# Kernel tuning notes

Hardware: AMD Instinct MI355X
Metric: run time of the kernel (lower is better)

Reference implementation:

```python
import jax, jax.numpy as jnp
import numpy as np
import math

E = 4096  # embed_dim
H = 32    # num_heads
M = 256   # max_queries
B = 8     # batch
N = 256   # kv tokens (16x16 grid -> no pos-embed interpolation branch)


def _sincos_1d(d, pos):
    omega = np.arange(d // 2, dtype=np.float32) / (d / 2.0)
    omega = 1.0 / 10000 ** omega
    out = np.einsum('m,d->md', pos.reshape(-1), omega)
    return np.concatenate([np.sin(out), np.cos(out)], axis=1)


def _sincos_2d(embed_dim, grid_size):
    gh = np.arange(grid_size, dtype=np.float32)
    gw = np.arange(grid_size, dtype=np.float32)
    grid = np.stack(np.meshgrid(gw, gh), axis=0).reshape(2, -1)
    return np.concatenate([
        _sincos_1d(embed_dim // 2, grid[0]),
        _sincos_1d(embed_dim // 2, grid[1]),
    ], axis=1)


def setup_inputs() -> dict:
    key = jax.random.key(0)
    ks = jax.random.split(key, 4)
    grid_size = int(math.ceil(math.sqrt(M)))
    pe = _sincos_2d(E, grid_size)[:M].astype(np.float32)
    return {
        'x': jax.random.normal(ks[0], (B, N, E), jnp.float32),
        'query': 0.02 * jax.random.normal(ks[1], (M, E), jnp.float32),
        'pos_embed': jnp.asarray(pe),
        'ln_q_w': jnp.ones((E,), jnp.float32),
        'ln_q_b': jnp.zeros((E,), jnp.float32),
        'ln_kv_w': jnp.ones((E,), jnp.float32),
        'ln_kv_b': jnp.zeros((E,), jnp.float32),
        'in_proj_w': 0.02 * jax.random.normal(ks[2], (3 * E, E), jnp.float32),
        'in_proj_b': jnp.zeros((3 * E,), jnp.float32),
        'out_proj_w': 0.02 * jax.random.normal(ks[3], (E, E), jnp.float32),
        'out_proj_b': jnp.zeros((E,), jnp.float32),
    }


def _ln(x, w, b, eps=1e-5):
    m = jnp.mean(x, -1, keepdims=True)
    v = jnp.mean((x - m) ** 2, -1, keepdims=True)
    return (x - m) * jax.lax.rsqrt(v + eps) * w + b


def reference(x, query, pos_embed, ln_q_w, ln_q_b, ln_kv_w, ln_kv_b,
              in_proj_w, in_proj_b, out_proj_w, out_proj_b):
    D = E // H
    kv = _ln(x, ln_kv_w, ln_kv_b)                      # [B,N,E] (kv_proj is Identity)
    q_in = _ln(query, ln_q_w, ln_q_b) + pos_embed      # [M,E] (Q + posQ, shared over batch)
    k_in = kv + pos_embed[None]                        # N == M so posK == pos_embed (no interp)
    Wq, Wk, Wv = in_proj_w[:E], in_proj_w[E:2 * E], in_proj_w[2 * E:]
    bq, bk, bv = in_proj_b[:E], in_proj_b[E:2 * E], in_proj_b[2 * E:]
    q = (q_in @ Wq.T + bq).reshape(M, H, D).transpose(1, 0, 2)          # [H,M,D]
    k = (k_in @ Wk.T + bk).reshape(B, N, H, D).transpose(0, 2, 1, 3)    # [B,H,N,D]
    v = (kv @ Wv.T + bv).reshape(B, N, H, D).transpose(0, 2, 1, 3)      # [B,H,N,D]
    scores = jnp.einsum('hmd,bhnd->bhmn', q, k) / jnp.sqrt(jnp.float32(D))
    attn = jax.nn.softmax(scores, axis=-1)                              # [B,H,M,N]
    o = jnp.einsum('bhmn,bhnd->bhmd', attn, v)
    o = o.transpose(0, 2, 1, 3).reshape(B, M, E)
    out = o @ out_proj_w.T + out_proj_b                                 # [B,M,E]
    # need_weights=True with average_attn_weights=True -> head-averaged weights
    return out, attn.mean(axis=1)
```

## Files before the change

kernel.cpp:

```cpp
#include <hip/hip_runtime.h>
#include <hip/hip_bf16.h>

typedef __bf16 bf16;
typedef __attribute__((ext_vector_type(8))) __bf16 bf16x8;
typedef __attribute__((ext_vector_type(4))) __bf16 bf16x4;
typedef __attribute__((ext_vector_type(4))) float floatx4;

#define E_DIM 4096
#define H_DIM 32
#define D_DIM 128
#define M_DIM 256
#define B_DIM 8
#define N_DIM 256

#define GLD_LDS(g, l) __builtin_amdgcn_global_load_lds( \
    (const __attribute__((address_space(1))) unsigned int*)(g), \
    (__attribute__((address_space(3))) unsigned int*)(l), 16, 0, 0)

__device__ __forceinline__ float wave_sum(float v) {
#pragma unroll
  for (int o = 32; o; o >>= 1) v += __shfl_xor(v, o);
  return v;
}
__device__ __forceinline__ float wave_max(float v) {
#pragma unroll
  for (int o = 32; o; o >>= 1) v = fmaxf(v, __shfl_xor(v, o));
  return v;
}

#define BAR256() asm volatile("s_barrier" ::: "memory")
#define LGKM0_256()                                      \
  asm volatile("s_waitcnt lgkmcnt(0)" ::: "memory");     \
  __builtin_amdgcn_sched_barrier(0)

#define STAGE_A256(T, h)                                                       \
  {                                                                            \
    _Pragma("unroll") for (int j = 0; j < 2; ++j)                              \
        GLD_LDS(Ag + (size_t)((h)*128 + sgrow + j * 8) * lda + (T) * 64 + sgcol, \
                AsP + ((T)&1) * 16384 + (h)*8192 + sdst + j * 512);            \
  }
#define STAGE_B256(T, h)                                                       \
  {                                                                            \
    _Pragma("unroll") for (int j = 0; j < 2; ++j)                              \
        GLD_LDS(Bg + (size_t)((h)*128 + sgrow + j * 8) * ldb + (T) * 64 + sgcol, \
                BsP + ((T)&1) * 16384 + (h)*8192 + sdst + j * 512);            \
  }
#define LDA256(mh)                                                             \
  {                                                                            \
    _Pragma("unroll") for (int m = 0; m < 4; ++m) {                            \
      a[m][0] = *(const bf16x8*)(AsP + buf + rA + ((mh)*4 + m) * 1024 + slot0); \
      a[m][1] = *(const bf16x8*)(AsP + buf + rA + ((mh)*4 + m) * 1024 + slot1); \
    }                                                                          \
  }
#define LDB256(dst, nh)                                                        \
  {                                                                            \
    _Pragma("unroll") for (int n = 0; n < 2; ++n) {                            \
      dst[n][0] = *(const bf16x8*)(BsP + buf + rB + ((nh)*2 + n) * 1024 + slot0); \
      dst[n][1] = *(const bf16x8*)(BsP + buf + rB + ((nh)*2 + n) * 1024 + slot1); \
    }                                                                          \
  }
#define MFMAQ(mb, nb, B)                                                       \
  {                                                                            \
    _Pragma("unroll") for (int m = 0; m < 4; ++m)                              \
        _Pragma("unroll") for (int n = 0; n < 2; ++n) {                        \
      acc[(mb) + m][(nb) + n] = __builtin_amdgcn_mfma_f32_16x16x32_bf16(       \
          a[m][0], B[n][0], acc[(mb) + m][(nb) + n], 0, 0, 0);                 \
      acc[(mb) + m][(nb) + n] = __builtin_amdgcn_mfma_f32_16x16x32_bf16(       \
          a[m][1], B[n][1], acc[(mb) + m][(nb) + n], 0, 0, 0);                 \
    }                                                                          \
  }

__device__ __forceinline__ void gemm256_core(const bf16* __restrict__ Ag,
                                             const bf16* __restrict__ Bg,
                                             int lda, int ldb, int nkt,
                                             bf16* AsP, bf16* BsP,
                                             floatx4 (&acc)[8][4],
                                             int wid, int lane) {
  const int wm = wid >> 2, wn = wid & 3;
  const int l15 = lane & 15, q = lane >> 4, e7 = lane & 7;
  const int slot0 = ((q ^ e7) & 7) * 8;
  const int slot1 = (((4 + q) ^ e7) & 7) * 8;
  const int rA = (wm * 128 + l15) * 64;
  const int rB = (wn * 64 + l15) * 64;
  const int sgrow = wid * 16 + (lane >> 3);
  const int sgcol = ((lane & 7) ^ (lane >> 3)) * 8;
  const int sdst = wid * 1024;

  bf16x8 a[4][2], b0[2][2], b1[2][2];

  STAGE_B256(0, 0); STAGE_B256(0, 1);
  STAGE_A256(0, 0); STAGE_A256(0, 1);
  STAGE_B256(1, 0); STAGE_B256(1, 1);

  for (int U = 0; U < nkt; ++U) {
    const int buf = (U & 1) * 16384;
    if (U + 1 < nkt)
      asm volatile("s_waitcnt vmcnt(4)\n\ts_barrier" ::: "memory");
    else
      asm volatile("s_waitcnt vmcnt(0)\n\ts_barrier" ::: "memory");
    LDA256(0); LDB256(b0, 0);
    if (U + 1 < nkt) { STAGE_A256(U + 1, 0); }
    BAR256(); LGKM0_256();
    __builtin_amdgcn_s_setprio(1); MFMAQ(0, 0, b0); __builtin_amdgcn_s_setprio(0);
    __builtin_amdgcn_sched_barrier(0); BAR256();
    LDB256(b1, 1);
    if (U + 1 < nkt) { STAGE_A256(U + 1, 1); }
    BAR256(); LGKM0_256();
    __builtin_amdgcn_s_setprio(1); MFMAQ(0, 2, b1); __builtin_amdgcn_s_setprio(0);
    __builtin_amdgcn_sched_barrier(0); BAR256();
    LDA256(1);
    if (U + 2 < nkt) { STAGE_B256(U + 2, 0); }
    BAR256(); LGKM0_256();
    __builtin_amdgcn_s_setprio(1); MFMAQ(4, 2, b1); __builtin_amdgcn_s_setprio(0);
    __builtin_amdgcn_sched_barrier(0); BAR256();
    if (U + 2 < nkt) { STAGE_B256(U + 2, 1); }
    BAR256();
    __builtin_amdgcn_s_setprio(1); MFMAQ(4, 0, b0); __builtin_amdgcn_s_setprio(0);
    __builtin_amdgcn_sched_barrier(0);
  }
}

__global__ __launch_bounds__(512, 1)
void proj256(const bf16* __restrict__ qin, const bf16* __restrict__ kin,
             const bf16* __restrict__ kv, const bf16* __restrict__ Wqkv,
             const float* __restrict__ bqkv, float* __restrict__ qpart,
             bf16* __restrict__ kp, bf16* __restrict__ vt) {
  __shared__ __align__(16) bf16 As2[32768];
  __shared__ __align__(16) bf16 Bs2[32768];
  const int tid = threadIdx.x, wid = tid >> 6, lane = tid & 63;

  const int o = blockIdx.x;
  const int id = (o & 7) * 32 + (o >> 3);
  int role, bx, by;
  const bf16 *A, *B;
  const float* bias;
  bf16* C;
  if (id < 128) {
    role = 1; by = id & 7; bx = id >> 3;
    A = kin; B = Wqkv + 16777216; bias = bqkv + 4096; C = kp;
  } else {
    role = 2; by = (id - 128) & 7; bx = (id - 128) >> 3;
    A = kv; B = Wqkv + 33554432; bias = bqkv + 8192; C = vt;
  }
  const int trowA = by * 256, trowB = bx * 256;
  const bf16* Ag = A + (size_t)trowA * E_DIM;
  const bf16* Bg = B + (size_t)trowB * E_DIM;

  floatx4 acc[8][4];
#pragma unroll
  for (int i = 0; i < 8; ++i)
#pragma unroll
    for (int j = 0; j < 4; ++j) acc[i][j] = (floatx4){0.f, 0.f, 0.f, 0.f};

  gemm256_core(Ag, Bg, E_DIM, E_DIM, 64, As2, Bs2, acc, wid, lane);

  const int wm = wid >> 2, wn = wid & 3;
  const int l15 = lane & 15, q = lane >> 4;
  const int mrow0 = trowA + wm * 128 + q * 4;
  const int ncol0 = trowB + wn * 64 + l15;
  if (role == 1) {
#pragma unroll
    for (int m = 0; m < 8; ++m)
#pragma unroll
      for (int n = 0; n < 4; ++n) {
        const int col = ncol0 + n * 16;
        const float bb = bias[col];
        floatx4 v = acc[m][n];
#pragma unroll
        for (int r = 0; r < 4; ++r)
          C[(size_t)(mrow0 + m * 16 + r) * E_DIM + col] = (bf16)(v[r] + bb);
      }
  } else {
#pragma unroll
    for (int m = 0; m < 8; ++m)
#pragma unroll
      for (int n = 0; n < 4; ++n) {
        const int col = ncol0 + n * 16;
        const int h = col >> 7, d = col & 127;
        const float bb = bias[col];
        const int row0 = mrow0 + m * 16;
        const int b_ = row0 >> 8, n_ = row0 & 255;
        floatx4 v = acc[m][n];
        bf16x4 p;
#pragma unroll
        for (int r = 0; r < 4; ++r) p[r] = (bf16)(v[r] + bb);
        *(bf16x4*)(C + ((size_t)((b_ * H_DIM + h) * D_DIM + d)) * N_DIM + n_) = p;
      }
  }

  const int qx = id & 15, kc = id >> 4;
  const bf16* Agq = qin + kc * 256;
  const bf16* Bgq = Wqkv + (size_t)(qx * 256) * E_DIM + kc * 256;
#pragma unroll
  for (int i = 0; i < 8; ++i)
#pragma unroll
    for (int j = 0; j < 4; ++j) acc[i][j] = (floatx4){0.f, 0.f, 0.f, 0.f};

  gemm256_core(Agq, Bgq, E_DIM, E_DIM, 4, As2, Bs2, acc, wid, lane);

  float* qdst = qpart + (size_t)kc * 1048576;
  const int qmrow0 = wm * 128 + q * 4;
  const int qncol0 = qx * 256 + wn * 64 + l15;
#pragma unroll
  for (int m = 0; m < 8; ++m)
#pragma unroll
    for (int n = 0; n < 4; ++n) {
      const int col = qncol0 + n * 16;
      floatx4 v = acc[m][n];
#pragma unroll
      for (int r = 0; r < 4; ++r)
        qdst[(size_t)(qmrow0 + m * 16 + r) * E_DIM + col] = v[r];
    }
}

__global__ __launch_bounds__(256) void qreduce_kernel(const float* __restrict__ qpart,
                                                      const float* __restrict__ bias,
                                                      bf16* __restrict__ qp) {
  const size_t i = ((size_t)blockIdx.x * 256 + threadIdx.x) * 4;
  float4 s = *(const float4*)(bias + (i & 4095));
#pragma unroll
  for (int kc = 0; kc < 16; ++kc) {
    float4 v = *(const float4*)(qpart + (size_t)kc * 1048576 + i);
    s.x += v.x; s.y += v.y; s.z += v.z; s.w += v.w;
  }
  bf16x4 p; p[0] = (bf16)s.x; p[1] = (bf16)s.y; p[2] = (bf16)s.z; p[3] = (bf16)s.w;
  *(bf16x4*)(qp + i) = p;
}

__global__ __launch_bounds__(512, 1)
void outproj256(const bf16* __restrict__ obuf, const bf16* __restrict__ Wout,
                float* __restrict__ Cf) {
  __shared__ __align__(16) bf16 As2[32768];
  __shared__ __align__(16) bf16 Bs2[32768];
  const int tid = threadIdx.x, wid = tid >> 6, lane = tid & 63;

  const int o = blockIdx.x;
  const int id = (o & 7) * 32 + (o >> 3);
  const int z = id >> 7;
  const int t = id & 127;
  const int by = t & 7, bx = t >> 3;
  const int trowA = by * 256, trowB = bx * 256;
  const bf16* Ag = obuf + (size_t)z * 2048 + (size_t)trowA * E_DIM;
  const bf16* Bg = Wout + (size_t)z * 2048 + (size_t)trowB * E_DIM;

  floatx4 acc[8][4];
#pragma unroll
  for (int i = 0; i < 8; ++i)
#pragma unroll
    for (int j = 0; j < 4; ++j) acc[i][j] = (floatx4){0.f, 0.f, 0.f, 0.f};

  gemm256_core(Ag, Bg, E_DIM, E_DIM, 32, As2, Bs2, acc, wid, lane);

  const int wm = wid >> 2, wn = wid & 3;
  const int l15 = lane & 15, q = lane >> 4;
  const int mrow0 = trowA + wm * 128 + q * 4;
  const int ncol0 = trowB + wn * 64 + l15;
#pragma unroll
  for (int m = 0; m < 8; ++m)
#pragma unroll
    for (int n = 0; n < 4; ++n) {
      const int col = ncol0 + n * 16;
      floatx4 v = acc[m][n];
#pragma unroll
      for (int r = 0; r < 4; ++r)
        Cf[(size_t)z * 8388608 + (size_t)(mrow0 + m * 16 + r) * E_DIM + col] = v[r];
    }
}

__device__ __forceinline__ void gemm_core_small(const bf16* __restrict__ Arow,
                                                const bf16* __restrict__ Brow,
                                                int lda, int ldb, int kTiles,
                                                bf16* As, bf16* Bs,
                                                floatx4 (&acc)[4][4],
                                                int wid, int lane) {
  const int s0 = wid * 2;
  const int lp = lane ^ ((lane >> 3) & 7);
  const int srow = lp >> 2;
  const int skoff = (lp & 3) * 8;
  const int rA = (wid >> 1) * 64 + (lane & 15);
  const int rB = (wid & 1) * 64 + (lane & 15);
  const int q16 = (lane >> 4) * 8;
  const int ex = (((lane & 15) >> 1) & 7) << 3;

#pragma unroll
  for (int c = 0; c < 2; ++c) {
    const int s = s0 + c;
    const int row = s * 16 + srow;
    GLD_LDS(Arow + (size_t)row * lda + skoff, As + s * 512);
    GLD_LDS(Brow + (size_t)row * ldb + skoff, Bs + s * 512);
  }

  for (int kt = 0; kt < kTiles; ++kt) {
    const int cur = (kt & 1) * 4096;
    const int nxt = 4096 - cur;
    __syncthreads();
    if (kt + 1 < kTiles) {
      const int k0 = (kt + 1) << 5;
#pragma unroll
      for (int c = 0; c < 2; ++c) {
        const int s = s0 + c;
        const int row = s * 16 + srow;
        GLD_LDS(Arow + (size_t)row * lda + k0 + skoff, As + nxt + s * 512);
        GLD_LDS(Brow + (size_t)row * ldb + k0 + skoff, Bs + nxt + s * 512);
      }
    }
    bf16x8 af[4], bfr[4];
#pragma unroll
    for (int t = 0; t < 4; ++t) {
      af[t] = *(const bf16x8*)(As + cur + ((((rA + t * 16) * 32) + q16) ^ ex));
      bfr[t] = *(const bf16x8*)(Bs + cur + ((((rB + t * 16) * 32) + q16) ^ ex));
    }
#pragma unroll
    for (int tr = 0; tr < 4; ++tr)
#pragma unroll
      for (int tc = 0; tc < 4; ++tc)
        acc[tr][tc] = __builtin_amdgcn_mfma_f32_16x16x32_bf16(af[tr], bfr[tc],
                                                              acc[tr][tc], 0, 0, 0);
  }
}

__global__ __launch_bounds__(256) void cvt_all_kernel(const float* __restrict__ s1,
                                                      bf16* __restrict__ d1,
                                                      const float* __restrict__ s2,
                                                      bf16* __restrict__ d2) {
  long i = ((long)blockIdx.x * 256 + threadIdx.x) * 8;
  const float* src;
  bf16* dst;
  if (i < 50331648L) { src = s1 + i; dst = d1 + i; }
  else { src = s2 + (i - 50331648L); dst = d2 + (i - 50331648L); }
  float4 a = *(const float4*)(src);
  float4 b = *(const float4*)(src + 4);
  bf16x8 p;
  p[0] = (bf16)a.x; p[1] = (bf16)a.y; p[2] = (bf16)a.z; p[3] = (bf16)a.w;
  p[4] = (bf16)b.x; p[5] = (bf16)b.y; p[6] = (bf16)b.z; p[7] = (bf16)b.w;
  *(bf16x8*)(dst) = p;
}

__global__ __launch_bounds__(256) void ln_x_kernel(const float* __restrict__ x,
                                                   const float* __restrict__ w,
                                                   const float* __restrict__ bvec,
                                                   const float* __restrict__ pos,
                                                   bf16* __restrict__ kv,
                                                   bf16* __restrict__ kin) {
  const int row = blockIdx.x;
  const int n = row & (N_DIM - 1);
  const int tid = threadIdx.x, wid = tid >> 6, lane = tid & 63;
  const float* xr = x + (size_t)row * E_DIM;
  float4 v[4];
  float s1 = 0.f, s2 = 0.f;
#pragma unroll
  for (int j = 0; j < 4; ++j) {
    v[j] = *(const float4*)(xr + j * 1024 + tid * 4);
    s1 += v[j].x + v[j].y + v[j].z + v[j].w;
    s2 += v[j].x * v[j].x + v[j].y * v[j].y + v[j].z * v[j].z + v[j].w * v[j].w;
  }
  s1 = wave_sum(s1); s2 = wave_sum(s2);
  __shared__ float red[8];
  if (lane == 0) { red[wid] = s1; red[wid + 4] = s2; }
  __syncthreads();
  s1 = red[0] + red[1] + red[2] + red[3];
  s2 = red[4] + red[5] + red[6] + red[7];
  const float mean = s1 * (1.f / E_DIM);
  const float var = s2 * (1.f / E_DIM) - mean * mean;
  const float rs = rsqrtf(var + 1e-5f);
#pragma unroll
  for (int j = 0; j < 4; ++j) {
    const int idx = j * 1024 + tid * 4;
    float4 wv = *(const float4*)(w + idx);
    float4 bv = *(const float4*)(bvec + idx);
    float4 pv = *(const float4*)(pos + (size_t)n * E_DIM + idx);
    float y0 = (v[j].x - mean) * rs * wv.x + bv.x;
    float y1 = (v[j].y - mean) * rs * wv.y + bv.y;
    float y2 = (v[j].z - mean) * rs * wv.z + bv.z;
    float y3 = (v[j].w - mean) * rs * wv.w + bv.w;
    bf16x4 a; a[0] = (bf16)y0; a[1] = (bf16)y1; a[2] = (bf16)y2; a[3] = (bf16)y3;
    *(bf16x4*)(kv + (size_t)row * E_DIM + idx) = a;
    bf16x4 c; c[0] = (bf16)(y0 + pv.x); c[1] = (bf16)(y1 + pv.y);
    c[2] = (bf16)(y2 + pv.z); c[3] = (bf16)(y3 + pv.w);
    *(bf16x4*)(kin + (size_t)row * E_DIM + idx) = c;
  }
}

__global__ __launch_bounds__(256) void ln_q_kernel(const float* __restrict__ q,
                                                   const float* __restrict__ w,
                                                   const float* __restrict__ bvec,
                                                   const float* __restrict__ pos,
                                                   bf16* __restrict__ qin) {
  const int row = blockIdx.x;
  const int tid = threadIdx.x, wid = tid >> 6, lane = tid & 63;
  const float* xr = q + (size_t)row * E_DIM;
  float4 v[4];
  float s1 = 0.f, s2 = 0.f;
#pragma unroll
  for (int j = 0; j < 4; ++j) {
    v[j] = *(const float4*)(xr + j * 1024 + tid * 4);
    s1 += v[j].x + v[j].y + v[j].z + v[j].w;
    s2 += v[j].x * v[j].x + v[j].y * v[j].y + v[j].z * v[j].z + v[j].w * v[j].w;
  }
  s1 = wave_sum(s1); s2 = wave_sum(s2);
  __shared__ float red[8];
  if (lane == 0) { red[wid] = s1; red[wid + 4] = s2; }
  __syncthreads();
  s1 = red[0] + red[1] + red[2] + red[3];
  s2 = red[4] + red[5] + red[6] + red[7];
  const float mean = s1 * (1.f / E_DIM);
  const float var = s2 * (1.f / E_DIM) - mean * mean;
  const float rs = rsqrtf(var + 1e-5f);
#pragma unroll
  for (int j = 0; j < 4; ++j) {
    const int idx = j * 1024 + tid * 4;
    float4 wv = *(const float4*)(w + idx);
    float4 bv = *(const float4*)(bvec + idx);
    float4 pv = *(const float4*)(pos + (size_t)row * E_DIM + idx);
    bf16x4 a;
    a[0] = (bf16)((v[j].x - mean) * rs * wv.x + bv.x + pv.x);
    a[1] = (bf16)((v[j].y - mean) * rs * wv.y + bv.y + pv.y);
    a[2] = (bf16)((v[j].z - mean) * rs * wv.z + bv.z + pv.z);
    a[3] = (bf16)((v[j].w - mean) * rs * wv.w + bv.w + pv.w);
    *(bf16x4*)(qin + (size_t)row * E_DIM + idx) = a;
  }
}

template <int MODE>
__global__ __launch_bounds__(256, 2)
void gemm_bt(const bf16* __restrict__ Abase, const bf16* __restrict__ Bbase,
             float* __restrict__ Cf, bf16* __restrict__ Cb,
             int K, int lda, int ldb, int ldc, float scale) {
  __shared__ __align__(16) bf16 As[8192];
  __shared__ __align__(16) bf16 Bs[8192];
  const int tid = threadIdx.x;
  const int wid = tid >> 6;
  const int lane = tid & 63;

  const bf16* A = Abase;
  const bf16* B = Bbase;
  if constexpr (MODE == 2) {
    int z = blockIdx.z; int zb = z >> 5, zh = z & 31;
    A += zh * D_DIM;
    B += ((size_t)zb * N_DIM) * E_DIM + zh * D_DIM;
  } else if constexpr (MODE == 3) {
    int z = blockIdx.z;
    A += (size_t)z * M_DIM * 512;
    B += (size_t)z * D_DIM * N_DIM;
  }

  const bf16* Arow = A + (size_t)(blockIdx.y * 128) * lda;
  const bf16* Brow = B + (size_t)(blockIdx.x * 128) * ldb;

  floatx4 acc[4][4];
#pragma unroll
  for (int i = 0; i < 4; ++i)
#pragma unroll
    for (int j = 0; j < 4; ++j) acc[i][j] = (floatx4){0.f, 0.f, 0.f, 0.f};

  gemm_core_small(Arow, Brow, lda, ldb, K >> 5, As, Bs, acc, wid, lane);

  const int mb = blockIdx.y * 128 + (wid >> 1) * 64 + (lane >> 4) * 4;
  const int nb = blockIdx.x * 128 + (wid & 1) * 64 + (lane & 15);
#pragma unroll
  for (int tr = 0; tr < 4; ++tr) {
#pragma unroll
    for (int tc = 0; tc < 4; ++tc) {
      const int row0 = mb + tr * 16;
      const int col = nb + tc * 16;
      floatx4 a = acc[tr][tc];
      if constexpr (MODE == 2) {
#pragma unroll
        for (int r = 0; r < 4; ++r)
          Cf[(size_t)blockIdx.z * (M_DIM * N_DIM) + (size_t)(row0 + r) * ldc + col] =
              a[r] * scale;
      } else {
        int z = blockIdx.z; int zb_ = z >> 5, zh_ = z & 31;
#pragma unroll
        for (int r = 0; r < 4; ++r)
          Cb[(size_t)zb_ * M_DIM * E_DIM + (size_t)(row0 + r) * E_DIM + zh_ * D_DIM + col] =
              (bf16)a[r];
      }
    }
  }
}

__global__ __launch_bounds__(256) void reduce_out_kernel(const float* __restrict__ p,
                                                         const float* __restrict__ bias,
                                                         float* __restrict__ out) {
  const size_t i = ((size_t)blockIdx.x * 256 + threadIdx.x) * 4;
  float4 a = *(const float4*)(p + i);
  float4 b = *(const float4*)(p + 8388608 + i);
  float4 bb = *(const float4*)(bias + (i & 4095));
  float4 o;
  o.x = a.x + b.x + bb.x; o.y = a.y + b.y + bb.y;
  o.z = a.z + b.z + bb.z; o.w = a.w + b.w + bb.w;
  *(float4*)(out + i) = o;
}

__global__ __launch_bounds__(256) void softmax_mean_kernel(float* __restrict__ scores,
                                                           float* __restrict__ out_mean) {
  const int bm = blockIdx.x;
  const int b = bm >> 8, m = bm & 255;
  const int wid = threadIdx.x >> 6, lane = threadIdx.x & 63;
  float a0 = 0.f, a1 = 0.f, a2 = 0.f, a3 = 0.f;
  for (int j = 0; j < 8; ++j) {
    const int h = wid * 8 + j;
    float* row = scores + ((size_t)((b * H_DIM + h) * M_DIM + m)) * N_DIM;
    float4 v = *(const float4*)(row + lane * 4);
    float mx = fmaxf(fmaxf(v.x, v.y), fmaxf(v.z, v.w));
    mx = wave_max(mx);
    v.x = __expf(v.x - mx); v.y = __expf(v.y - mx);
    v.z = __expf(v.z - mx); v.w = __expf(v.w - mx);
    const float s = wave_sum(v.x + v.y + v.z + v.w);
    const float inv = 1.f / s;
    v.x *= inv; v.y *= inv; v.z *= inv; v.w *= inv;
    a0 += v.x; a1 += v.y; a2 += v.z; a3 += v.w;
    bf16x4 p; p[0] = (bf16)v.x; p[1] = (bf16)v.y; p[2] = (bf16)v.z; p[3] = (bf16)v.w;
    *(bf16x4*)((bf16*)row + lane * 4) = p;
  }
  __shared__ float red[4][256];
  *(float4*)&red[wid][lane * 4] = make_float4(a0, a1, a2, a3);
  __syncthreads();
  if (wid == 0) {
    float4 r0 = *(float4*)&red[0][lane * 4];
    float4 r1 = *(float4*)&red[1][lane * 4];
    float4 r2 = *(float4*)&red[2][lane * 4];
    float4 r3 = *(float4*)&red[3][lane * 4];
    float4 o;
    o.x = (r0.x + r1.x + r2.x + r3.x) * (1.f / H_DIM);
    o.y = (r0.y + r1.y + r2.y + r3.y) * (1.f / H_DIM);
    o.z = (r0.z + r1.z + r2.z + r3.z) * (1.f / H_DIM);
    o.w = (r0.w + r1.w + r2.w + r3.w) * (1.f / H_DIM);
    *(float4*)(out_mean + (size_t)bm * N_DIM + lane * 4) = o;
  }
}

extern "C" void kernel_launch(void* const* d_in, const int* in_sizes, int n_in,
                              void* d_out, int out_size, void* d_ws, size_t ws_size,
                              hipStream_t stream) {
  const float* x = (const float*)d_in[0];
  const float* query = (const float*)d_in[1];
  const float* pos = (const float*)d_in[2];
  const float* ln_q_w = (const float*)d_in[3];
  const float* ln_q_b = (const float*)d_in[4];
  const float* ln_kv_w = (const float*)d_in[5];
  const float* ln_kv_b = (const float*)d_in[6];
  const float* Wqkv_f = (const float*)d_in[7];
  const float* bqkv = (const float*)d_in[8];
  const float* Wout_f = (const float*)d_in[9];
  const float* bout = (const float*)d_in[10];

  char* ws = (char*)d_ws;
  bf16* Wqkv = (bf16*)(ws + 0);
  bf16* Wout = (bf16*)(ws + 100663296);
  bf16* kv   = (bf16*)(ws + 134217728);
  bf16* kin  = (bf16*)(ws + 150994944);
  bf16* qin  = (bf16*)(ws + 167772160);
  bf16* qp   = (bf16*)(ws + 169869312);
  bf16* kp   = (bf16*)(ws + 171966464);
  bf16* vt   = (bf16*)(ws + 188743680);
  float* partials = (float*)(ws + 205520896);
  float* qpart = partials;
  float* scores = (float*)(ws + 0);
  bf16* obuf = (bf16*)(ws + 67108864);

  float* out = (float*)d_out;
  float* out2 = out + (size_t)B_DIM * M_DIM * E_DIM;

  cvt_all_kernel<<<32768, 256, 0, stream>>>(Wqkv_f, Wqkv, Wout_f, Wout);
  ln_x_kernel<<<2048, 256, 0, stream>>>(x, ln_kv_w, ln_kv_b, pos, kv, kin);
  ln_q_kernel<<<256, 256, 0, stream>>>(query, ln_q_w, ln_q_b, pos, qin);

  proj256<<<256, 512, 0, stream>>>(qin, kin, kv, Wqkv, bqkv, qpart, kp, vt);
  qreduce_kernel<<<1024, 256, 0, stream>>>(qpart, bqkv, qp);

  gemm_bt<2><<<dim3(2, 2, 256), 256, 0, stream>>>(qp, kp, scores, nullptr,
                                                  128, 4096, 4096, 256,
                                                  0.08838834764831845f);
  softmax_mean_kernel<<<2048, 256, 0, stream>>>(scores, out2);
  gemm_bt<3><<<dim3(1, 2, 256), 256, 0, stream>>>((const bf16*)scores, vt,
                                                  nullptr, obuf,
                                                  256, 512, 256, 4096, 1.f);
  outproj256<<<256, 512, 0, stream>>>(obuf, Wout, partials);
  reduce_out_kernel<<<8192, 256, 0, stream>>>(partials, bout, out);
}
```

Measured before the change: 732.6 us.

## Fuse weight conversion and layernorms into one prep kernel; use 256-tile scores GEMM

Merges the fp32-to-bf16 weight conversion and both layernorm kernels into a single prep launch, where conversion blocks each handle 8 chunks. It also replaces the 128x128 gemm_bt scores kernel (1024 blocks) with a 256x256-tile kernel, one block per batch-head, built on the existing gemm256_core. This cuts launch count and lets the small LN work overlap with the conversion. The larger tile improves operand reuse but drops to 256 blocks with one block per CU, so occupancy is lower.

```diff
diff --git a/kernel.cpp b/kernel.cpp
--- a/kernel.cpp
+++ b/kernel.cpp
@@ -228,6 +228,44 @@
 }
 
 __global__ __launch_bounds__(512, 1)
+void scores256(const bf16* __restrict__ qp, const bf16* __restrict__ kp,
+               float* __restrict__ scores, float scale) {
+  __shared__ __align__(16) bf16 As2[32768];
+  __shared__ __align__(16) bf16 Bs2[32768];
+  const int tid = threadIdx.x, wid = tid >> 6, lane = tid & 63;
+
+  const int o = blockIdx.x;
+  const int z = (o & 7) * 32 + (o >> 3);
+  const int zb = z >> 5, zh = z & 31;
+  const bf16* Ag = qp + zh * D_DIM;
+  const bf16* Bg = kp + (size_t)zb * N_DIM * E_DIM + zh * D_DIM;
+
+  floatx4 acc[8][4];
+#pragma unroll
+  for (int i = 0; i < 8; ++i)
+#pragma unroll
+    for (int j = 0; j < 4; ++j) acc[i][j] = (floatx4){0.f, 0.f, 0.f, 0.f};
+
+  gemm256_core(Ag, Bg, E_DIM, E_DIM, 2, As2, Bs2, acc, wid, lane);
+
+  const int wm = wid >> 2, wn = wid & 3;
+  const int l15 = lane & 15, q = lane >> 4;
+  const int mrow0 = wm * 128 + q * 4;
+  const int ncol0 = wn * 64 + l15;
+  float* Cz = scores + (size_t)z * (M_DIM * N_DIM);
+#pragma unroll
+  for (int m = 0; m < 8; ++m)
+#pragma unroll
+    for (int n = 0; n < 4; ++n) {
+      const int col = ncol0 + n * 16;
+      floatx4 v = acc[m][n];
+#pragma unroll
+      for (int r = 0; r < 4; ++r)
+        Cz[(size_t)(mrow0 + m * 16 + r) * N_DIM + col] = v[r] * scale;
+    }
+}
+
+__global__ __launch_bounds__(512, 1)
 void outproj256(const bf16* __restrict__ obuf, const bf16* __restrict__ Wout,
                 float* __restrict__ Cf) {
   __shared__ __align__(16) bf16 As2[32768];
@@ -319,33 +357,43 @@
   }
 }
 
-__global__ __launch_bounds__(256) void cvt_all_kernel(const float* __restrict__ s1,
-                                                      bf16* __restrict__ d1,
-                                                      const float* __restrict__ s2,
-                                                      bf16* __restrict__ d2) {
-  long i = ((long)blockIdx.x * 256 + threadIdx.x) * 8;
-  const float* src;
-  bf16* dst;
-  if (i < 50331648L) { src = s1 + i; dst = d1 + i; }
-  else { src = s2 + (i - 50331648L); dst = d2 + (i - 50331648L); }
-  float4 a = *(const float4*)(src);
-  float4 b = *(const float4*)(src + 4);
-  bf16x8 p;
-  p[0] = (bf16)a.x; p[1] = (bf16)a.y; p[2] = (bf16)a.z; p[3] = (bf16)a.w;
-  p[4] = (bf16)b.x; p[5] = (bf16)b.y; p[6] = (bf16)b.z; p[7] = (bf16)b.w;
-  *(bf16x8*)(dst) = p;
-}
-
-__global__ __launch_bounds__(256) void ln_x_kernel(const float* __restrict__ x,
-                                                   const float* __restrict__ w,
-                                                   const float* __restrict__ bvec,
-                                                   const float* __restrict__ pos,
-                                                   bf16* __restrict__ kv,
-                                                   bf16* __restrict__ kin) {
-  const int row = blockIdx.x;
-  const int n = row & (N_DIM - 1);
+__global__ __launch_bounds__(256) void prep_kernel(
+    const float* __restrict__ x, const float* __restrict__ lnxw,
+    const float* __restrict__ lnxb, const float* __restrict__ pos,
+    bf16* __restrict__ kv, bf16* __restrict__ kin,
+    const float* __restrict__ qsrc, const float* __restrict__ lnqw,
+    const float* __restrict__ lnqb, bf16* __restrict__ qin,
+    const float* __restrict__ Wqkv_f, bf16* __restrict__ Wqkv,
+    const float* __restrict__ Wout_f, bf16* __restrict__ Wout) {
+  const int bid = blockIdx.x;
   const int tid = threadIdx.x, wid = tid >> 6, lane = tid & 63;
-  const float* xr = x + (size_t)row * E_DIM;
+
+  if (bid >= 2304) {
+    const int cb = bid - 2304;
+#pragma unroll
+    for (int c = 0; c < 8; ++c) {
+      long i = (((long)c * 4096 + cb) * 256 + tid) * 8;
+      const float* src;
+      bf16* dst;
+      if (i < 50331648L) { src = Wqkv_f + i; dst = Wqkv + i; }
+      else { src = Wout_f + (i - 50331648L); dst = Wout + (i - 50331648L); }
+      float4 a = *(const float4*)(src);
+      float4 b = *(const float4*)(src + 4);
+      bf16x8 p;
+      p[0] = (bf16)a.x; p[1] = (bf16)a.y; p[2] = (bf16)a.z; p[3] = (bf16)a.w;
+      p[4] = (bf16)b.x; p[5] = (bf16)b.y; p[6] = (bf16)b.z; p[7] = (bf16)b.w;
+      *(bf16x8*)(dst) = p;
+    }
+    return;
+  }
+
+  const bool is_q = (bid >= 2048);
+  const int row = is_q ? (bid - 2048) : bid;
+  const float* xr = (is_q ? qsrc : x) + (size_t)row * E_DIM;
+  const float* w = is_q ? lnqw : lnxw;
+  const float* bvec = is_q ? lnqb : lnxb;
+  const int posrow = is_q ? row : (row & (N_DIM - 1));
+
   float4 v[4];
   float s1 = 0.f, s2 = 0.f;
 #pragma unroll
@@ -368,56 +416,23 @@
     const int idx = j * 1024 + tid * 4;
     float4 wv = *(const float4*)(w + idx);
     float4 bv = *(const float4*)(bvec + idx);
-    float4 pv = *(const float4*)(pos + (size_t)n * E_DIM + idx);
+    float4 pv = *(const float4*)(pos + (size_t)posrow * E_DIM + idx);
     float y0 = (v[j].x - mean) * rs * wv.x + bv.x;
     float y1 = (v[j].y - mean) * rs * wv.y + bv.y;
     float y2 = (v[j].z - mean) * rs * wv.z + bv.z;
     float y3 = (v[j].w - mean) * rs * wv.w + bv.w;
-    bf16x4 a; a[0] = (bf16)y0; a[1] = (bf16)y1; a[2] = (bf16)y2; a[3] = (bf16)y3;
-    *(bf16x4*)(kv + (size_t)row * E_DIM + idx) = a;
-    bf16x4 c; c[0] = (bf16)(y0 + pv.x); c[1] = (bf16)(y1 + pv.y);
-    c[2] = (bf16)(y2 + pv.z); c[3] = (bf16)(y3 + pv.w);
-    *(bf16x4*)(kin + (size_t)row * E_DIM + idx) = c;
-  }
-}
-
-__global__ __launch_bounds__(256) void ln_q_kernel(const float* __restrict__ q,
-                                                   const float* __restrict__ w,
-                                                   const float* __restrict__ bvec,
-                                                   const float* __restrict__ pos,
-                                                   bf16* __restrict__ qin) {
-  const int row = blockIdx.x;
-  const int tid = threadIdx.x, wid = tid >> 6, lane = tid & 63;
-  const float* xr = q + (size_t)row * E_DIM;
-  float4 v[4];
-  float s1 = 0.f, s2 = 0.f;
-#pragma unroll
-  for (int j = 0; j < 4; ++j) {
-    v[j] = *(const float4*)(xr + j * 1024 + tid * 4);
-    s1 += v[j].x + v[j].y + v[j].z + v[j].w;
-    s2 += v[j].x * v[j].x + v[j].y * v[j].y + v[j].z * v[j].z + v[j].w * v[j].w;
-  }
-  s1 = wave_sum(s1); s2 = wave_sum(s2);
-  __shared__ float red[8];
-  if (lane == 0) { red[wid] = s1; red[wid + 4] = s2; }
-  __syncthreads();
-  s1 = red[0] + red[1] + red[2] + red[3];
-  s2 = red[4] + red[5] + red[6] + red[7];
-  const float mean = s1 * (1.f / E_DIM);
-  const float var = s2 * (1.f / E_DIM) - mean * mean;
-  const float rs = rsqrtf(var + 1e-5f);
-#pragma unroll
-  for (int j = 0; j < 4; ++j) {
-    const int idx = j * 1024 + tid * 4;
-    float4 wv = *(const float4*)(w + idx);
-    float4 bv = *(const float4*)(bvec + idx);
-    float4 pv = *(const float4*)(pos + (size_t)row * E_DIM + idx);
-    bf16x4 a;
-    a[0] = (bf16)((v[j].x - mean) * rs * wv.x + bv.x + pv.x);
-    a[1] = (bf16)((v[j].y - mean) * rs * wv.y + bv.y + pv.y);
-    a[2] = (bf16)((v[j].z - mean) * rs * wv.z + bv.z + pv.z);
-    a[3] = (bf16)((v[j].w - mean) * rs * wv.w + bv.w + pv.w);
-    *(bf16x4*)(qin + (size_t)row * E_DIM + idx) = a;
+    if (is_q) {
+      bf16x4 a;
+      a[0] = (bf16)(y0 + pv.x); a[1] = (bf16)(y1 + pv.y);
+      a[2] = (bf16)(y2 + pv.z); a[3] = (bf16)(y3 + pv.w);
+      *(bf16x4*)(qin + (size_t)row * E_DIM + idx) = a;
+    } else {
+      bf16x4 a; a[0] = (bf16)y0; a[1] = (bf16)y1; a[2] = (bf16)y2; a[3] = (bf16)y3;
+      *(bf16x4*)(kv + (size_t)row * E_DIM + idx) = a;
+      bf16x4 c; c[0] = (bf16)(y0 + pv.x); c[1] = (bf16)(y1 + pv.y);
+      c[2] = (bf16)(y2 + pv.z); c[3] = (bf16)(y3 + pv.w);
+      *(bf16x4*)(kin + (size_t)row * E_DIM + idx) = c;
+    }
   }
 }
 
@@ -434,11 +449,7 @@
 
   const bf16* A = Abase;
   const bf16* B = Bbase;
-  if constexpr (MODE == 2) {
-    int z = blockIdx.z; int zb = z >> 5, zh = z & 31;
-    A += zh * D_DIM;
-    B += ((size_t)zb * N_DIM) * E_DIM + zh * D_DIM;
-  } else if constexpr (MODE == 3) {
+  if constexpr (MODE == 3) {
     int z = blockIdx.z;
     A += (size_t)z * M_DIM * 512;
     B += (size_t)z * D_DIM * N_DIM;
@@ -464,18 +475,11 @@
       const int row0 = mb + tr * 16;
       const int col = nb + tc * 16;
       floatx4 a = acc[tr][tc];
-      if constexpr (MODE == 2) {
-#pragma unroll
-        for (int r = 0; r < 4; ++r)
-          Cf[(size_t)blockIdx.z * (M_DIM * N_DIM) + (size_t)(row0 + r) * ldc + col] =
-              a[r] * scale;
-      } else {
-        int z = blockIdx.z; int zb_ = z >> 5, zh_ = z & 31;
-#pragma unroll
-        for (int r = 0; r < 4; ++r)
-          Cb[(size_t)zb_ * M_DIM * E_DIM + (size_t)(row0 + r) * E_DIM + zh_ * D_DIM + col] =
-              (bf16)a[r];
-      }
+      int z = blockIdx.z; int zb_ = z >> 5, zh_ = z & 31;
+#pragma unroll
+      for (int r = 0; r < 4; ++r)
+        Cb[(size_t)zb_ * M_DIM * E_DIM + (size_t)(row0 + r) * E_DIM + zh_ * D_DIM + col] =
+            (bf16)a[r];
     }
   }
 }
@@ -563,16 +567,14 @@
   float* out = (float*)d_out;
   float* out2 = out + (size_t)B_DIM * M_DIM * E_DIM;
 
-  cvt_all_kernel<<<32768, 256, 0, stream>>>(Wqkv_f, Wqkv, Wout_f, Wout);
-  ln_x_kernel<<<2048, 256, 0, stream>>>(x, ln_kv_w, ln_kv_b, pos, kv, kin);
-  ln_q_kernel<<<256, 256, 0, stream>>>(query, ln_q_w, ln_q_b, pos, qin);
+  prep_kernel<<<6400, 256, 0, stream>>>(x, ln_kv_w, ln_kv_b, pos, kv, kin,
+                                        query, ln_q_w, ln_q_b, qin,
+                                        Wqkv_f, Wqkv, Wout_f, Wout);
 
   proj256<<<256, 512, 0, stream>>>(qin, kin, kv, Wqkv, bqkv, qpart, kp, vt);
   qreduce_kernel<<<1024, 256, 0, stream>>>(qpart, bqkv, qp);
 
-  gemm_bt<2><<<dim3(2, 2, 256), 256, 0, stream>>>(qp, kp, scores, nullptr,
-                                                  128, 4096, 4096, 256,
-                                                  0.08838834764831845f);
+  scores256<<<256, 512, 0, stream>>>(qp, kp, scores, 0.08838834764831845f);
   softmax_mean_kernel<<<2048, 256, 0, stream>>>(scores, out2);
   gemm_bt<3><<<dim3(1, 2, 256), 256, 0, stream>>>((const bf16*)scores, vt,
                                                   nullptr, obuf,
```

New measurement: 736.9 us. About the same (+0.6%).
